# Optimization experiments

Measured on AMD Instinct MI355X. Metric: run time of the kernel, lower is better.

Reference implementation:

```python
import jax, jax.numpy as jnp
import numpy as np
import math

D_MODEL = 1024
NUM_HEADS = 16
D_HEAD = D_MODEL // NUM_HEADS  # 64
B, S = 2, 1024


def setup_inputs() -> dict:
    key = jax.random.key(0)
    ks = jax.random.split(key, 11)
    s = 1.0 / math.sqrt(D_MODEL)
    inp = {
        "Q": jax.random.normal(ks[0], (B, S, D_MODEL), jnp.float32),
        "K": jax.random.normal(ks[1], (B, S, D_MODEL), jnp.float32),
        "V": jax.random.normal(ks[2], (B, S, D_MODEL), jnp.float32),
        "Wq": jax.random.normal(ks[3], (D_MODEL, D_MODEL), jnp.float32) * s,
        "bq": jnp.zeros((D_MODEL,), jnp.float32),
        "Wk": jax.random.normal(ks[4], (D_MODEL, D_MODEL), jnp.float32) * s,
        "bk": jnp.zeros((D_MODEL,), jnp.float32),
        "Wv": jax.random.normal(ks[5], (D_MODEL, D_MODEL), jnp.float32) * s,
        "bv": jnp.zeros((D_MODEL,), jnp.float32),
        "Wo": jax.random.normal(ks[6], (D_MODEL, D_MODEL), jnp.float32) * s,
        "bo": jnp.zeros((D_MODEL,), jnp.float32),
    }
    return inp


def _linear(x, W, b):
    # torch nn.Linear: x @ W.T + b
    return jnp.einsum("bsd,ed->bse", x, W) + b


def _split_heads(x):
    # Faithful to original: view(b, s, d_head, num_heads).transpose(1, 2)
    # -> 'heads' axis has size d_head, per-head dim is num_heads.
    b, s, _ = x.shape
    return x.reshape(b, s, D_HEAD, NUM_HEADS).transpose(0, 2, 1, 3)  # [b, d_head, s, num_heads]


def reference(Q, K, V, Wq, bq, Wk, bk, Wv, bv, Wo, bo):
    q = _split_heads(_linear(Q, Wq, bq))  # [b, h=d_head, s, e=num_heads]
    k = _split_heads(_linear(K, Wk, bk))
    v = _split_heads(_linear(V, Wv, bv))
    scale = 1.0 / math.sqrt(D_MODEL)  # original scales by sqrt(d_model)
    scores = jnp.einsum("bhqe,bhke->bhqk", q, k) * scale
    attn = jax.nn.softmax(scores, axis=-1)
    ctx = jnp.einsum("bhqk,bhke->bhqe", attn, v)  # [b, d_head, s, num_heads]
    # combine_heads: transpose(1,2) then flatten last two dims
    b, h, s, e = ctx.shape
    merged = ctx.transpose(0, 2, 1, 3).reshape(b, s, h * e)
    return _linear(merged, Wo, bo)
```

## Files before the change

### kernel.cpp

```cpp
#include <hip/hip_runtime.h>
#include <cstdint>
#include <cstddef>
#include <math.h>

typedef _Float16 f16;
typedef _Float16 f16x8 __attribute__((ext_vector_type(8)));
typedef _Float16 f16x4 __attribute__((ext_vector_type(4)));
typedef float f32x4 __attribute__((ext_vector_type(4)));
typedef float f32x16 __attribute__((ext_vector_type(16)));

#define MFMA16(A, B, C) __builtin_amdgcn_mfma_f32_16x16x32_f16((A), (B), (C), 0, 0, 0)
#define MFMA32(A, B, C) __builtin_amdgcn_mfma_f32_32x32x16_f16((A), (B), (C), 0, 0, 0)

#if __has_builtin(__builtin_amdgcn_exp2f)
#define EXP2(x) __builtin_amdgcn_exp2f(x)
#else
#define EXP2(x) exp2f(x)
#endif

__device__ __forceinline__ f16x8 ld8(const f16* p) { return *(const f16x8*)p; }
__device__ __forceinline__ void st8(f16* p, f16x8 v) { *(f16x8*)p = v; }
__device__ __forceinline__ void st4(f16* p, f16x4 v) { *(f16x4*)p = v; }

__device__ __forceinline__ void gll16(const f16* g, f16* l) {
    __builtin_amdgcn_global_load_lds(
        (__attribute__((address_space(1))) void*)(uintptr_t)g,
        (__attribute__((address_space(3))) void*)(unsigned)(uintptr_t)l,
        16, 0, 0);
}

__global__ __launch_bounds__(256) void cast_all(
    const float* __restrict__ Q, const float* __restrict__ K, const float* __restrict__ V,
    const float* __restrict__ Wq, const float* __restrict__ Wk, const float* __restrict__ Wv,
    const float* __restrict__ Wo, f16* __restrict__ dst)
{
    size_t e = ((size_t)blockIdx.x * 256 + threadIdx.x) * 8;
    const float* s; size_t r;
    if (e < 2097152)      { s = Q;  r = e; }
    else if (e < 4194304) { s = K;  r = e - 2097152; }
    else if (e < 6291456) { s = V;  r = e - 4194304; }
    else if (e < 7340032) { s = Wq; r = e - 6291456; }
    else if (e < 8388608) { s = Wk; r = e - 7340032; }
    else if (e < 9437184) { s = Wv; r = e - 8388608; }
    else                  { s = Wo; r = e - 9437184; }
    float4 a = *(const float4*)(s + r);
    float4 b = *(const float4*)(s + r + 4);
    f16x8 o;
    o[0]=(f16)a.x; o[1]=(f16)a.y; o[2]=(f16)a.z; o[3]=(f16)a.w;
    o[4]=(f16)b.x; o[5]=(f16)b.y; o[6]=(f16)b.z; o[7]=(f16)b.w;
    st8(dst + e, o);
}

__global__ __launch_bounds__(256) void qkv_gemm(
    const f16* __restrict__ ws, const float* __restrict__ bq,
    const float* __restrict__ bk, const float* __restrict__ bv,
    f16* __restrict__ outbase)
{
    const int bx = blockIdx.x, bm = blockIdx.y;
    const int mat = bx >> 4, bn = bx & 15;
    const f16* A  = ws + (size_t)mat * 2097152;
    const f16* Bw = ws + 6291456 + (size_t)mat * 1048576;
    const float* bias = (mat == 0) ? bq : (mat == 1) ? bk : bv;
    f16* C = outbase + (size_t)mat * 2097152;

    __shared__ f16 As[4096], Bs[2048];
    const int t = threadIdx.x;
    const int w = t >> 6, lane = t & 63, lg = lane >> 4, ll = lane & 15;
    const int wm = w * 32;

    const f16* Ap = A  + (size_t)(bm * 128 + (t >> 2)) * 1024 + (t & 3) * 8;
    const f16* Bp = Bw + (size_t)(bn * 64  + (t >> 2)) * 1024 + (t & 3) * 8;
    f16* Asw = As + w * 512;
    f16* Bsw = Bs + w * 512;

    f32x4 acc[2][4] = {};

    for (int k0 = 0; k0 < 1024; k0 += 32) {
        __syncthreads();
        gll16(Ap + k0,         Asw);
        gll16(Ap + k0 + 65536, Asw + 2048);
        gll16(Bp + k0,         Bsw);
        __syncthreads();
        f16x8 af[2], bf[4];
        #pragma unroll
        for (int x = 0; x < 2; ++x)
            af[x] = ld8(&As[(wm + x * 16 + ll) * 32 + lg * 8]);
        #pragma unroll
        for (int y = 0; y < 4; ++y)
            bf[y] = ld8(&Bs[(y * 16 + ll) * 32 + lg * 8]);
        #pragma unroll
        for (int i = 0; i < 2; ++i)
            #pragma unroll
            for (int j = 0; j < 4; ++j)
                acc[i][j] = MFMA16(af[i], bf[j], acc[i][j]);
    }

    const int r0 = bm * 128 + wm + lg * 4;
    const int c0 = bn * 64 + ll;
    if (mat < 2) {
        #pragma unroll
        for (int j = 0; j < 4; ++j) {
            const float bv_ = bias[c0 + j * 16];
            #pragma unroll
            for (int i = 0; i < 2; ++i)
                #pragma unroll
                for (int r = 0; r < 4; ++r)
                    C[(size_t)(r0 + i * 16 + r) * 1024 + c0 + j * 16] = (f16)(acc[i][j][r] + bv_);
        }
    } else {
        #pragma unroll
        for (int j = 0; j < 4; ++j) {
            const int c = c0 + j * 16;
            const float bv_ = bias[c];
            #pragma unroll
            for (int i = 0; i < 2; ++i) {
                const int m0 = r0 + i * 16;
                const int bb = m0 >> 10, s0 = m0 & 1023;
                f16x4 pv;
                pv[0] = (f16)(acc[i][j][0] + bv_);
                pv[1] = (f16)(acc[i][j][1] + bv_);
                pv[2] = (f16)(acc[i][j][2] + bv_);
                pv[3] = (f16)(acc[i][j][3] + bv_);
                st4(C + ((size_t)((bb * 64 + (c >> 4)) * 16 + (c & 15))) * 1024 + s0, pv);
            }
        }
    }
}

__global__ __launch_bounds__(256, 4) void attn(
    const f16* __restrict__ qlin, const f16* __restrict__ klin,
    const f16* __restrict__ vT, f16* __restrict__ merged)
{
    __shared__ f16 Ks[128 * 16];
    __shared__ f16 Vs[16 * 136];
    __shared__ f16 Ps[4 * 32 * 40];

    const int t = threadIdx.x;
    const int w = t >> 6, lane = t & 63;
    const int l5 = lane & 31, hh = lane >> 5, lg = (lane >> 4) & 3, ll = lane & 15;
    const int h = blockIdx.x, qt = blockIdx.y, b = blockIdx.z;

    const int rowQ0 = b * 1024 + qt * 128;
    const int colh = h * 16;

    f16x8 qf = ld8(qlin + (size_t)(rowQ0 + w * 32 + l5) * 1024 + colh + hh * 8);

    float lsum = 0.f;
    f32x4 O0 = {}, O1 = {};
    f16* Pw = Ps + w * 1280;
    const float csc = 0.04508422002778009f;

    const f16* kbase = klin + (size_t)(b * 1024 + w * 32 + (lane >> 1)) * 1024 + colh + (lane & 1) * 8;
    f16* Ksw = Ks + w * 512;
    const int ve = t >> 4, vk = (t & 15) * 8;
    const f16* vbase = vT + (size_t)((b * 64 + h) * 16 + ve) * 1024 + vk;
    f16* vdst = &Vs[ve * 136 + vk];

    for (int kt = 0; kt < 8; ++kt) {
        __syncthreads();
        gll16(kbase + (size_t)kt * 131072, Ksw);
        st8(vdst, ld8(vbase + kt * 128));
        __syncthreads();

        #pragma unroll
        for (int mt = 0; mt < 4; ++mt) {
            f16x8 ka = ld8(&Ks[(mt * 32 + l5) * 16 + hh * 8]);
            f32x16 Sz = {};
            f32x16 S = MFMA32(ka, qf, Sz);

            #pragma unroll
            for (int g = 0; g < 4; ++g) {
                float p0 = EXP2(S[4 * g + 0] * csc);
                float p1 = EXP2(S[4 * g + 1] * csc);
                float p2 = EXP2(S[4 * g + 2] * csc);
                float p3 = EXP2(S[4 * g + 3] * csc);
                lsum += (p0 + p1) + (p2 + p3);
                f16x4 pk;
                pk[0] = (f16)p0; pk[1] = (f16)p1; pk[2] = (f16)p2; pk[3] = (f16)p3;
                st4(&Pw[l5 * 40 + g * 8 + hh * 4], pk);
            }

            f16x8 va  = ld8(&Vs[ll * 136 + mt * 32 + lg * 8]);
            f16x8 pb0 = ld8(&Pw[ll * 40 + lg * 8]);
            f16x8 pb1 = ld8(&Pw[(16 + ll) * 40 + lg * 8]);
            O0 = MFMA16(va, pb0, O0);
            O1 = MFMA16(va, pb1, O1);
        }
    }

    lsum += __shfl_xor(lsum, 32);
    const float i0 = 1.f / __shfl(lsum, ll);
    const float i1 = 1.f / __shfl(lsum, 16 + ll);

    f16x4 o0, o1;
    o0[0]=(f16)(O0[0]*i0); o0[1]=(f16)(O0[1]*i0); o0[2]=(f16)(O0[2]*i0); o0[3]=(f16)(O0[3]*i0);
    o1[0]=(f16)(O1[0]*i1); o1[1]=(f16)(O1[1]*i1); o1[2]=(f16)(O1[2]*i1); o1[3]=(f16)(O1[3]*i1);
    const size_t q0 = rowQ0 + w * 32 + ll;
    st4(merged + q0 * 1024 + colh + lg * 4, o0);
    st4(merged + (q0 + 16) * 1024 + colh + lg * 4, o1);
}

__global__ __launch_bounds__(256) void o_gemm(
    const f16* __restrict__ A, const f16* __restrict__ Bw,
    const float* __restrict__ bias, float* __restrict__ Cf)
{
    const int bn = blockIdx.x, bm = blockIdx.y;
    __shared__ f16 As[4096], Bs[2048];
    const int t = threadIdx.x;
    const int w = t >> 6, lane = t & 63, lg = lane >> 4, ll = lane & 15;
    const int wm = w * 32;

    const f16* Ap = A  + (size_t)(bm * 128 + (t >> 2)) * 1024 + (t & 3) * 8;
    const f16* Bp = Bw + (size_t)(bn * 64  + (t >> 2)) * 1024 + (t & 3) * 8;
    f16* Asw = As + w * 512;
    f16* Bsw = Bs + w * 512;

    f32x4 acc[2][4] = {};

    for (int k0 = 0; k0 < 1024; k0 += 32) {
        __syncthreads();
        gll16(Ap + k0,         Asw);
        gll16(Ap + k0 + 65536, Asw + 2048);
        gll16(Bp + k0,         Bsw);
        __syncthreads();
        f16x8 af[2], bf[4];
        #pragma unroll
        for (int x = 0; x < 2; ++x)
            af[x] = ld8(&As[(wm + x * 16 + ll) * 32 + lg * 8]);
        #pragma unroll
        for (int y = 0; y < 4; ++y)
            bf[y] = ld8(&Bs[(y * 16 + ll) * 32 + lg * 8]);
        #pragma unroll
        for (int i = 0; i < 2; ++i)
            #pragma unroll
            for (int j = 0; j < 4; ++j)
                acc[i][j] = MFMA16(af[i], bf[j], acc[i][j]);
    }

    const int r0 = bm * 128 + wm + lg * 4;
    const int c0 = bn * 64 + ll;
    #pragma unroll
    for (int j = 0; j < 4; ++j) {
        const float bv_ = bias[c0 + j * 16];
        #pragma unroll
        for (int i = 0; i < 2; ++i)
            #pragma unroll
            for (int r = 0; r < 4; ++r)
                Cf[(size_t)(r0 + i * 16 + r) * 1024 + c0 + j * 16] = acc[i][j][r] + bv_;
    }
}

extern "C" void kernel_launch(void* const* d_in, const int* in_sizes, int n_in,
                              void* d_out, int out_size, void* d_ws, size_t ws_size,
                              hipStream_t stream) {
    (void)in_sizes; (void)n_in; (void)out_size; (void)ws_size;
    const float* Q  = (const float*)d_in[0];
    const float* K  = (const float*)d_in[1];
    const float* V  = (const float*)d_in[2];
    const float* Wq = (const float*)d_in[3];
    const float* bq = (const float*)d_in[4];
    const float* Wk = (const float*)d_in[5];
    const float* bk = (const float*)d_in[6];
    const float* Wv = (const float*)d_in[7];
    const float* bv = (const float*)d_in[8];
    const float* Wo = (const float*)d_in[9];
    const float* bo = (const float*)d_in[10];
    float* out = (float*)d_out;

    f16* ws = (f16*)d_ws;
    f16* qlin   = ws + 10485760;
    f16* klin   = ws + 12582912;
    f16* vT     = ws + 14680064;
    f16* merged = ws + 16777216;
    f16* Woc    = ws + 9437184;

    cast_all<<<5120, 256, 0, stream>>>(Q, K, V, Wq, Wk, Wv, Wo, ws);
    qkv_gemm<<<dim3(48, 16), 256, 0, stream>>>(ws, bq, bk, bv, qlin);
    attn<<<dim3(64, 8, 2), 256, 0, stream>>>(qlin, klin, vT, merged);
    o_gemm<<<dim3(16, 16), 256, 0, stream>>>(merged, Woc, bo, out);
}
```

Before: 171.3 us.

## Double-buffer GEMM and attention tiles, swizzle LDS, fold softmax scale into Q

Both GEMMs now run with a K-step of 64 and double-buffered shared-memory tiles, prefetching the next tile during the current MFMA work, which removes one barrier per step. They also use an XOR-swizzled LDS layout to avoid bank conflicts, and their tile shapes change (64x128 for QKV, 64x64 for the O projection). The attention kernel double-buffers its K/V tiles with a swizzled K layout. The softmax scale is folded into the Q projection epilogue, so the exp loop no longer multiplies by it. The cost is more LDS per block, which may lower occupancy, and some added index arithmetic.

```diff
diff --git a/kernel.cpp b/kernel.cpp
--- a/kernel.cpp
+++ b/kernel.cpp
@@ -57,71 +57,98 @@
     f16* __restrict__ outbase)
 {
     const int bx = blockIdx.x, bm = blockIdx.y;
-    const int mat = bx >> 4, bn = bx & 15;
+    const int mat = bx >> 3, bn = bx & 7;
     const f16* A  = ws + (size_t)mat * 2097152;
     const f16* Bw = ws + 6291456 + (size_t)mat * 1048576;
     const float* bias = (mat == 0) ? bq : (mat == 1) ? bk : bv;
     f16* C = outbase + (size_t)mat * 2097152;
 
-    __shared__ f16 As[4096], Bs[2048];
+    __shared__ f16 As[2 * 4096];
+    __shared__ f16 Bs[2 * 8192];
     const int t = threadIdx.x;
     const int w = t >> 6, lane = t & 63, lg = lane >> 4, ll = lane & 15;
-    const int wm = w * 32;
-
-    const f16* Ap = A  + (size_t)(bm * 128 + (t >> 2)) * 1024 + (t & 3) * 8;
-    const f16* Bp = Bw + (size_t)(bn * 64  + (t >> 2)) * 1024 + (t & 3) * 8;
-    f16* Asw = As + w * 512;
-    f16* Bsw = Bs + w * 512;
-
-    f32x4 acc[2][4] = {};
-
-    for (int k0 = 0; k0 < 1024; k0 += 32) {
+    const int swz = ((lane & 7) ^ (lane >> 3)) * 8;
+
+    const f16* Ap = A  + (size_t)(bm * 64  + w * 8 + (lane >> 3)) * 1024 + swz;
+    const f16* Bp = Bw + (size_t)(bn * 128 + w * 8 + (lane >> 3)) * 1024 + swz;
+
+    f32x4 acc[4][2] = {};
+    const int ll7 = ll & 7;
+
+    {
+        gll16(Ap,         &As[w * 512]);
+        gll16(Ap + 32768, &As[2048 + w * 512]);
+        #pragma unroll
+        for (int q = 0; q < 4; ++q)
+            gll16(Bp + q * 32768, &Bs[q * 2048 + w * 512]);
+    }
+
+    #pragma unroll 2
+    for (int kt = 0; kt < 16; ++kt) {
+        const int cur = kt & 1;
         __syncthreads();
-        gll16(Ap + k0,         Asw);
-        gll16(Ap + k0 + 65536, Asw + 2048);
-        gll16(Bp + k0,         Bsw);
-        __syncthreads();
-        f16x8 af[2], bf[4];
-        #pragma unroll
-        for (int x = 0; x < 2; ++x)
-            af[x] = ld8(&As[(wm + x * 16 + ll) * 32 + lg * 8]);
-        #pragma unroll
-        for (int y = 0; y < 4; ++y)
-            bf[y] = ld8(&Bs[(y * 16 + ll) * 32 + lg * 8]);
-        #pragma unroll
-        for (int i = 0; i < 2; ++i)
-            #pragma unroll
-            for (int j = 0; j < 4; ++j)
-                acc[i][j] = MFMA16(af[i], bf[j], acc[i][j]);
-    }
-
-    const int r0 = bm * 128 + wm + lg * 4;
-    const int c0 = bn * 64 + ll;
-    if (mat < 2) {
-        #pragma unroll
-        for (int j = 0; j < 4; ++j) {
-            const float bv_ = bias[c0 + j * 16];
-            #pragma unroll
-            for (int i = 0; i < 2; ++i)
+        if (kt < 15) {
+            const f16* Ak = Ap + (kt + 1) * 64;
+            const f16* Bk = Bp + (kt + 1) * 64;
+            f16* Ad = &As[(cur ^ 1) * 4096 + w * 512];
+            f16* Bd = &Bs[(cur ^ 1) * 8192 + w * 512];
+            gll16(Ak,         Ad);
+            gll16(Ak + 32768, Ad + 2048);
+            #pragma unroll
+            for (int q = 0; q < 4; ++q)
+                gll16(Bk + q * 32768, Bd + q * 2048);
+        }
+        const f16* Ac = &As[cur * 4096];
+        const f16* Bc = &Bs[cur * 8192];
+        #pragma unroll
+        for (int ks = 0; ks < 2; ++ks) {
+            f16x8 af[4], bf[2];
+            #pragma unroll
+            for (int i = 0; i < 4; ++i)
+                af[i] = ld8(&Ac[(i * 16 + ll) * 64 + (((ks * 4 + lg) ^ ll7) * 8)]);
+            #pragma unroll
+            for (int j = 0; j < 2; ++j)
+                bf[j] = ld8(&Bc[(w * 32 + j * 16 + ll) * 64 + (((ks * 4 + lg) ^ ll7) * 8)]);
+            #pragma unroll
+            for (int i = 0; i < 4; ++i)
+                #pragma unroll
+                for (int j = 0; j < 2; ++j)
+                    acc[i][j] = MFMA16(af[i], bf[j], acc[i][j]);
+        }
+    }
+
+    const float qscale = 0.04508422002778009f;
+    #pragma unroll
+    for (int j = 0; j < 2; ++j) {
+        const int n = bn * 128 + w * 32 + j * 16 + ll;
+        const float bv_ = bias[n];
+        if (mat == 0) {
+            #pragma unroll
+            for (int i = 0; i < 4; ++i) {
+                const int m0 = bm * 64 + i * 16 + lg * 4;
                 #pragma unroll
                 for (int r = 0; r < 4; ++r)
-                    C[(size_t)(r0 + i * 16 + r) * 1024 + c0 + j * 16] = (f16)(acc[i][j][r] + bv_);
-        }
-    } else {
-        #pragma unroll
-        for (int j = 0; j < 4; ++j) {
-            const int c = c0 + j * 16;
-            const float bv_ = bias[c];
-            #pragma unroll
-            for (int i = 0; i < 2; ++i) {
-                const int m0 = r0 + i * 16;
+                    C[(size_t)(m0 + r) * 1024 + n] = (f16)((acc[i][j][r] + bv_) * qscale);
+            }
+        } else if (mat == 1) {
+            #pragma unroll
+            for (int i = 0; i < 4; ++i) {
+                const int m0 = bm * 64 + i * 16 + lg * 4;
+                #pragma unroll
+                for (int r = 0; r < 4; ++r)
+                    C[(size_t)(m0 + r) * 1024 + n] = (f16)(acc[i][j][r] + bv_);
+            }
+        } else {
+            #pragma unroll
+            for (int i = 0; i < 4; ++i) {
+                const int m0 = bm * 64 + i * 16 + lg * 4;
                 const int bb = m0 >> 10, s0 = m0 & 1023;
                 f16x4 pv;
                 pv[0] = (f16)(acc[i][j][0] + bv_);
                 pv[1] = (f16)(acc[i][j][1] + bv_);
                 pv[2] = (f16)(acc[i][j][2] + bv_);
                 pv[3] = (f16)(acc[i][j][3] + bv_);
-                st4(C + ((size_t)((bb * 64 + (c >> 4)) * 16 + (c & 15))) * 1024 + s0, pv);
+                st4(C + ((size_t)((bb * 64 + (n >> 4)) * 16 + (n & 15))) * 1024 + s0, pv);
             }
         }
     }
@@ -131,9 +158,9 @@
     const f16* __restrict__ qlin, const f16* __restrict__ klin,
     const f16* __restrict__ vT, f16* __restrict__ merged)
 {
-    __shared__ f16 Ks[128 * 16];
-    __shared__ f16 Vs[16 * 136];
-    __shared__ f16 Ps[4 * 32 * 40];
+    __shared__ f16 Ks[2][2048];
+    __shared__ f16 Vs[2][2176];
+    __shared__ f16 Ps[4][1280];
 
     const int t = threadIdx.x;
     const int w = t >> 6, lane = t & 63;
@@ -145,42 +172,57 @@
 
     f16x8 qf = ld8(qlin + (size_t)(rowQ0 + w * 32 + l5) * 1024 + colh + hh * 8);
 
+    const int sp = ((lane & 7) - (lane >> 3)) & 7;
+    const f16* kptr = klin + (size_t)(b * 1024 + w * 32 + (lane >> 3) * 4 + (sp >> 1)) * 1024
+                      + colh + (sp & 1) * 8;
+    const int ve = t >> 4, vk = (t & 15) * 8;
+    const f16* vptr = vT + (size_t)((b * 64 + h) * 16 + ve) * 1024 + vk;
+    f16* vdst0 = &Vs[0][ve * 136 + vk];
+    f16* vdst1 = &Vs[1][ve * 136 + vk];
+
+    int offKa[4];
+    #pragma unroll
+    for (int mt = 0; mt < 4; ++mt) {
+        const int r = mt * 32 + l5, g = r >> 2;
+        offKa[mt] = g * 64 + (((((r & 3) * 2 + hh) + g) & 7) * 8);
+    }
+
     float lsum = 0.f;
     f32x4 O0 = {}, O1 = {};
-    f16* Pw = Ps + w * 1280;
-    const float csc = 0.04508422002778009f;
-
-    const f16* kbase = klin + (size_t)(b * 1024 + w * 32 + (lane >> 1)) * 1024 + colh + (lane & 1) * 8;
-    f16* Ksw = Ks + w * 512;
-    const int ve = t >> 4, vk = (t & 15) * 8;
-    const f16* vbase = vT + (size_t)((b * 64 + h) * 16 + ve) * 1024 + vk;
-    f16* vdst = &Vs[ve * 136 + vk];
+    f16* Pw = Ps[w];
+
+    f16x8 vv = ld8(vptr);
+    gll16(kptr, &Ks[0][w * 512]);
+    st8(vdst0, vv);
 
     for (int kt = 0; kt < 8; ++kt) {
+        const int cur = kt & 1;
+        if (kt < 7) vv = ld8(vptr + (kt + 1) * 128);
         __syncthreads();
-        gll16(kbase + (size_t)kt * 131072, Ksw);
-        st8(vdst, ld8(vbase + kt * 128));
-        __syncthreads();
+        if (kt < 7) {
+            gll16(kptr + (size_t)(kt + 1) * 131072, &Ks[cur ^ 1][w * 512]);
+            st8(cur ? vdst0 : vdst1, vv);
+        }
 
         #pragma unroll
         for (int mt = 0; mt < 4; ++mt) {
-            f16x8 ka = ld8(&Ks[(mt * 32 + l5) * 16 + hh * 8]);
+            f16x8 ka = ld8(&Ks[cur][offKa[mt]]);
             f32x16 Sz = {};
             f32x16 S = MFMA32(ka, qf, Sz);
 
             #pragma unroll
             for (int g = 0; g < 4; ++g) {
-                float p0 = EXP2(S[4 * g + 0] * csc);
-                float p1 = EXP2(S[4 * g + 1] * csc);
-                float p2 = EXP2(S[4 * g + 2] * csc);
-                float p3 = EXP2(S[4 * g + 3] * csc);
+                float p0 = EXP2(S[4 * g + 0]);
+                float p1 = EXP2(S[4 * g + 1]);
+                float p2 = EXP2(S[4 * g + 2]);
+                float p3 = EXP2(S[4 * g + 3]);
                 lsum += (p0 + p1) + (p2 + p3);
                 f16x4 pk;
                 pk[0] = (f16)p0; pk[1] = (f16)p1; pk[2] = (f16)p2; pk[3] = (f16)p3;
                 st4(&Pw[l5 * 40 + g * 8 + hh * 4], pk);
             }
 
-            f16x8 va  = ld8(&Vs[ll * 136 + mt * 32 + lg * 8]);
+            f16x8 va  = ld8(&Vs[cur][ll * 136 + mt * 32 + lg * 8]);
             f16x8 pb0 = ld8(&Pw[ll * 40 + lg * 8]);
             f16x8 pb1 = ld8(&Pw[(16 + ll) * 40 + lg * 8]);
             O0 = MFMA16(va, pb0, O0);
@@ -205,48 +247,62 @@
     const float* __restrict__ bias, float* __restrict__ Cf)
 {
     const int bn = blockIdx.x, bm = blockIdx.y;
-    __shared__ f16 As[4096], Bs[2048];
+    __shared__ f16 As[2 * 4096];
+    __shared__ f16 Bs[2 * 4096];
     const int t = threadIdx.x;
     const int w = t >> 6, lane = t & 63, lg = lane >> 4, ll = lane & 15;
-    const int wm = w * 32;
-
-    const f16* Ap = A  + (size_t)(bm * 128 + (t >> 2)) * 1024 + (t & 3) * 8;
-    const f16* Bp = Bw + (size_t)(bn * 64  + (t >> 2)) * 1024 + (t & 3) * 8;
-    f16* Asw = As + w * 512;
-    f16* Bsw = Bs + w * 512;
-
-    f32x4 acc[2][4] = {};
-
-    for (int k0 = 0; k0 < 1024; k0 += 32) {
+    const int swz = ((lane & 7) ^ (lane >> 3)) * 8;
+
+    const f16* Ap = A  + (size_t)(bm * 64 + w * 8 + (lane >> 3)) * 1024 + swz;
+    const f16* Bp = Bw + (size_t)(bn * 64 + w * 8 + (lane >> 3)) * 1024 + swz;
+
+    f32x4 acc[4] = {};
+    const int ll7 = ll & 7;
+
+    {
+        gll16(Ap,         &As[w * 512]);
+        gll16(Ap + 32768, &As[2048 + w * 512]);
+        gll16(Bp,         &Bs[w * 512]);
+        gll16(Bp + 32768, &Bs[2048 + w * 512]);
+    }
+
+    #pragma unroll 2
+    for (int kt = 0; kt < 16; ++kt) {
+        const int cur = kt & 1;
         __syncthreads();
-        gll16(Ap + k0,         Asw);
-        gll16(Ap + k0 + 65536, Asw + 2048);
-        gll16(Bp + k0,         Bsw);
-        __syncthreads();
-        f16x8 af[2], bf[4];
-        #pragma unroll
-        for (int x = 0; x < 2; ++x)
-            af[x] = ld8(&As[(wm + x * 16 + ll) * 32 + lg * 8]);
-        #pragma unroll
-        for (int y = 0; y < 4; ++y)
-            bf[y] = ld8(&Bs[(y * 16 + ll) * 32 + lg * 8]);
-        #pragma unroll
-        for (int i = 0; i < 2; ++i)
-            #pragma unroll
-            for (int j = 0; j < 4; ++j)
-                acc[i][j] = MFMA16(af[i], bf[j], acc[i][j]);
-    }
-
-    const int r0 = bm * 128 + wm + lg * 4;
-    const int c0 = bn * 64 + ll;
+        if (kt < 15) {
+            const f16* Ak = Ap + (kt + 1) * 64;
+            const f16* Bk = Bp + (kt + 1) * 64;
+            f16* Ad = &As[(cur ^ 1) * 4096 + w * 512];
+            f16* Bd = &Bs[(cur ^ 1) * 4096 + w * 512];
+            gll16(Ak,         Ad);
+            gll16(Ak + 32768, Ad + 2048);
+            gll16(Bk,         Bd);
+            gll16(Bk + 32768, Bd + 2048);
+        }
+        const f16* Ac = &As[cur * 4096];
+        const f16* Bc = &Bs[cur * 4096];
+        #pragma unroll
+        for (int ks = 0; ks < 2; ++ks) {
+            f16x8 af[4], bf;
+            #pragma unroll
+            for (int i = 0; i < 4; ++i)
+                af[i] = ld8(&Ac[(i * 16 + ll) * 64 + (((ks * 4 + lg) ^ ll7) * 8)]);
+            bf = ld8(&Bc[(w * 16 + ll) * 64 + (((ks * 4 + lg) ^ ll7) * 8)]);
+            #pragma unroll
+            for (int i = 0; i < 4; ++i)
+                acc[i] = MFMA16(af[i], bf, acc[i]);
+        }
+    }
+
+    const int n = bn * 64 + w * 16 + ll;
+    const float bv_ = bias[n];
     #pragma unroll
-    for (int j = 0; j < 4; ++j) {
-        const float bv_ = bias[c0 + j * 16];
-        #pragma unroll
-        for (int i = 0; i < 2; ++i)
-            #pragma unroll
-            for (int r = 0; r < 4; ++r)
-                Cf[(size_t)(r0 + i * 16 + r) * 1024 + c0 + j * 16] = acc[i][j][r] + bv_;
+    for (int i = 0; i < 4; ++i) {
+        const int m0 = bm * 64 + i * 16 + lg * 4;
+        #pragma unroll
+        for (int r = 0; r < 4; ++r)
+            Cf[(size_t)(m0 + r) * 1024 + n] = acc[i][r] + bv_;
     }
 }
 
@@ -275,7 +331,7 @@
     f16* Woc    = ws + 9437184;
 
     cast_all<<<5120, 256, 0, stream>>>(Q, K, V, Wq, Wk, Wv, Wo, ws);
-    qkv_gemm<<<dim3(48, 16), 256, 0, stream>>>(ws, bq, bk, bv, qlin);
+    qkv_gemm<<<dim3(24, 32), 256, 0, stream>>>(ws, bq, bk, bv, qlin);
     attn<<<dim3(64, 8, 2), 256, 0, stream>>>(qlin, klin, vT, merged);
-    o_gemm<<<dim3(16, 16), 256, 0, stream>>>(merged, Woc, bo, out);
-}
+    o_gemm<<<dim3(16, 32), 256, 0, stream>>>(merged, Woc, bo, out);
+}
```

Measured after the change: 159.8 us. -6.7%, faster.
